# Kernel optimization log

Hardware: AMD Instinct MI355X
Metric: run time of the kernel (lower is better)

The kernel has to match this reference:

```python
import jax, jax.numpy as jnp
import numpy as np

FACTOR = 5  # init factor


def setup_inputs() -> dict:
    key = jax.random.key(0)
    k1, k2, k3, k4 = jax.random.split(key, 4)
    B, H, L, D = 4, 8, 2048, 64
    sample_k = min(FACTOR * int(np.ceil(np.log(L))), L)  # 40
    queries = jax.random.normal(k1, (B, H, L, D), dtype=jnp.float32)
    keys = jax.random.normal(k2, (B, H, L, D), dtype=jnp.float32)
    values = jax.random.normal(k3, (B, H, L, D), dtype=jnp.float32)
    index_sample = jax.random.randint(k4, (L, sample_k), 0, L)
    return {"queries": queries, "keys": keys, "values": values,
            "index_sample": index_sample}


def reference(queries, keys, values, index_sample):
    B, H, L_Q, D = queries.shape
    L_K = keys.shape[2]
    n_top = min(FACTOR * int(np.ceil(np.log(L_Q))), L_Q)

    # --- _prob_QK ---
    # Gather sampled keys per query position: [B,H,L_Q,sample_k,D]
    K_sample = keys[:, :, index_sample, :]
    # Q.unsqueeze(3) @ K_sample^T -> [B,H,L_Q,sample_k]
    Q_K_sample = jnp.einsum('bhld,bhlsd->bhls', queries, K_sample)
    # sparsity measure M = max - mean
    M = Q_K_sample.max(axis=-1) - Q_K_sample.sum(axis=-1) / L_K
    _, M_top = jax.lax.top_k(M, n_top)  # [B,H,n_top]
    # gather top queries: [B,H,n_top,D]
    Q_reduce = jnp.take_along_axis(queries, M_top[..., None], axis=2)
    # full scores for top queries: [B,H,n_top,L_K]
    scores_top = jnp.einsum('bhud,bhkd->bhuk', Q_reduce, keys)

    # --- scale ---
    scale = 1.0 / np.sqrt(D).astype(np.float32)
    scores_top = scores_top * scale

    # --- initial context (mask_flag=False): mean of V broadcast over L_Q ---
    V_mean = values.mean(axis=2)  # [B,H,D]
    context = jnp.broadcast_to(V_mean[:, :, None, :], (B, H, L_Q, D))

    # --- update context at top-query positions ---
    attn = jax.nn.softmax(scores_top, axis=-1)           # [B,H,n_top,L_K]
    ctx_update = jnp.einsum('bhuk,bhkd->bhud', attn, values)
    b_idx = jnp.arange(B)[:, None, None]
    h_idx = jnp.arange(H)[None, :, None]
    context = context.at[b_idx, h_idx, M_top].set(ctx_update)
    return context
```

## Files before the change

kernel.cpp:

```cpp
#include <hip/hip_runtime.h>
#include <math.h>

#define BH 32
#define L  2048
#define D  64
#define SK 40
#define NT 40
#define NC 16
#define CK 128
#define SCALE 0.125f

#define WS_M      0
#define WS_MTOP   262144
#define WS_VP     267264
#define WS_VM     332800
#define WS_OPART  344064
#define WS_MPART  5586944
#define WS_LPART  5668864

__global__ __launch_bounds__(256) void kM(const float* __restrict__ Q,
                                          const float* __restrict__ K,
                                          const int* __restrict__ idx,
                                          float* __restrict__ M)
{
    __shared__ int sidx[16 * SK];
    int b    = blockIdx.x;
    int xcd  = b & 7;
    int slot = b >> 3;
    int head = (slot & 3) * 8 + xcd;
    int qc   = slot >> 2;
    int wave = threadIdx.x >> 6;
    int lane = threadIdx.x & 63;
    int qq   = lane >> 4;
    int dl   = lane & 15;

    int l0 = qc * 16;
    for (int i = threadIdx.x; i < 16 * SK; i += 256)
        sidx[i] = idx[(l0 + i / SK) * SK + (i % SK)];
    __syncthreads();

    int lq  = wave * 4 + qq;
    int l   = l0 + lq;
    int qid = head * L + l;

    float4 qv = reinterpret_cast<const float4*>(Q)[(size_t)qid * 16 + dl];
    const float4* K4 = reinterpret_cast<const float4*>(K) + (size_t)head * L * 16;

    float mx = -INFINITY, sm = 0.f;
    #pragma unroll 8
    for (int s = 0; s < SK; ++s) {
        int kr = sidx[lq * SK + s];
        float4 kv = K4[(size_t)kr * 16 + dl];
        float p = qv.x * kv.x + qv.y * kv.y + qv.z * kv.z + qv.w * kv.w;
        #pragma unroll
        for (int o = 1; o < 16; o <<= 1) p += __shfl_xor(p, o, 64);
        mx = fmaxf(mx, p);
        sm += p;
    }
    if (dl == 0) M[qid] = mx - sm * (1.0f / (float)L);
}

__global__ __launch_bounds__(256) void kTop(const float* __restrict__ M, int* __restrict__ Mtop)
{
    __shared__ unsigned int keys[L];
    __shared__ int hist[256];
    __shared__ int ssum[256];
    __shared__ int bsel;
    __shared__ unsigned int pref_s;
    __shared__ int krem_s;
    __shared__ int cnt_gt, cnt_eq;
    __shared__ int eqlist[64];

    int bh = blockIdx.x;
    int t  = threadIdx.x;

    for (int i = t; i < L; i += 256) {
        unsigned int u = __float_as_uint(M[bh * L + i]);
        keys[i] = (u & 0x80000000u) ? ~u : (u | 0x80000000u);
    }
    if (t == 0) { pref_s = 0u; krem_s = NT; cnt_gt = 0; cnt_eq = 0; }
    __syncthreads();

    #pragma unroll
    for (int shift = 24; shift >= 0; shift -= 8) {
        hist[t] = 0;
        __syncthreads();
        unsigned int pref = pref_s;
        for (int i = t; i < L; i += 256) {
            unsigned int k  = keys[i];
            unsigned int hi = (shift == 24) ? 0u : (k >> (shift + 8));
            if (hi == pref) atomicAdd(&hist[(k >> shift) & 0xFF], 1);
        }
        __syncthreads();
        ssum[t] = hist[t];
        __syncthreads();
        for (int st = 1; st < 256; st <<= 1) {
            int v = (t + st < 256) ? ssum[t + st] : 0;
            __syncthreads();
            ssum[t] += v;
            __syncthreads();
        }
        int krem = krem_s;
        int excl = ssum[t] - hist[t];
        if (excl < krem && excl + hist[t] >= krem) bsel = t;
        __syncthreads();
        if (t == 0) {
            int bb = bsel;
            krem_s = krem_s - (ssum[bb] - hist[bb]);
            pref_s = (pref_s << 8) | (unsigned int)bb;
        }
        __syncthreads();
    }

    unsigned int T = pref_s;
    int krem = krem_s;
    for (int i = t; i < L; i += 256) {
        unsigned int k = keys[i];
        if (k > T) {
            int p = atomicAdd(&cnt_gt, 1);
            Mtop[bh * NT + p] = i;
        } else if (k == T) {
            int p = atomicAdd(&cnt_eq, 1);
            if (p < 64) eqlist[p] = i;
        }
    }
    __syncthreads();
    if (t == 0) {
        int base = cnt_gt;
        int m = cnt_eq < 64 ? cnt_eq : 64;
        for (int q = 0; q < krem; ++q) {
            int best = 0x7fffffff, bj = -1;
            for (int j = 0; j < m; ++j) if (eqlist[j] < best) { best = eqlist[j]; bj = j; }
            Mtop[bh * NT + base + q] = best;
            if (bj >= 0) eqlist[bj] = 0x7fffffff;
        }
    }
}

__global__ __launch_bounds__(256) void kVmean1(const float* __restrict__ V,
                                               float* __restrict__ Vp)
{
    __shared__ float red[256];
    int b  = blockIdx.x;
    int bh = b >> 3, c = b & 7;
    int dl = threadIdx.x & 63;
    int g  = threadIdx.x >> 6;
    const float* Vb = V + (size_t)bh * L * D;
    float acc = 0.f;
    int base = c * 256 + g * 64;
    for (int k = 0; k < 64; ++k) acc += Vb[(size_t)(base + k) * D + dl];
    red[threadIdx.x] = acc;
    __syncthreads();
    if (threadIdx.x < 64)
        Vp[b * 64 + dl] = red[dl] + red[64 + dl] + red[128 + dl] + red[192 + dl];
}

__global__ __launch_bounds__(64) void kVmean2(const float* __restrict__ Vp,
                                              float* __restrict__ Vm)
{
    int bh = blockIdx.x, d = threadIdx.x;
    float s = 0.f;
    #pragma unroll
    for (int c = 0; c < 8; ++c) s += Vp[(bh * 8 + c) * 64 + d];
    Vm[bh * D + d] = s * (1.0f / (float)L);
}

__global__ __launch_bounds__(256) void kFill(const float* __restrict__ Vm,
                                             float* __restrict__ out)
{
    int tid  = blockIdx.x * 256 + threadIdx.x;
    int base = tid * 4;
    int bh   = base >> 17;
    int d0   = base & (D - 1);
    float4 v = *reinterpret_cast<const float4*>(Vm + bh * D + d0);
    *reinterpret_cast<float4*>(out + base) = v;
}

__global__ __launch_bounds__(256, 2) void kAttnPart(const float* __restrict__ Q,
                                                    const float* __restrict__ K,
                                                    const float* __restrict__ V,
                                                    const int* __restrict__ Mtop,
                                                    float* __restrict__ Opart,
                                                    float* __restrict__ mpart,
                                                    float* __restrict__ lpart)
{
    __shared__ float4 KV4[CK * 16];
    __shared__ float4 Qs4[NT * 16];
    __shared__ float  S[NT * CK];
    __shared__ int    mrow[NT];
    __shared__ float  smax[NT], ssum[NT];

    int c = blockIdx.x, bh = blockIdx.y;
    int t = threadIdx.x;

    if (t < NT) mrow[t] = Mtop[bh * NT + t];
    __syncthreads();

    const float4* Qg = reinterpret_cast<const float4*>(Q) + (size_t)bh * L * 16;
    for (int i = t; i < NT * 16; i += 256) {
        int u = i >> 4, d4 = i & 15;
        Qs4[i] = Qg[(size_t)mrow[u] * 16 + d4];
    }
    const float4* Kg = reinterpret_cast<const float4*>(K) + ((size_t)bh * L + c * CK) * 16;
    for (int i = t; i < CK * 16; i += 256) {
        int j = i >> 4, d4 = i & 15;
        KV4[j * 16 + (d4 ^ (j & 15))] = Kg[i];
    }
    __syncthreads();

    {
        int wave = t >> 6, lane = t & 63;
        int jh = wave & 1, uh = wave >> 1;
        int j = jh * 64 + lane;
        float4 k4[16];
        #pragma unroll
        for (int d4 = 0; d4 < 16; ++d4) k4[d4] = KV4[j * 16 + (d4 ^ (j & 15))];
        for (int u = uh * 20; u < uh * 20 + 20; ++u) {
            float acc = 0.f;
            #pragma unroll
            for (int d4 = 0; d4 < 16; ++d4) {
                float4 q4 = Qs4[u * 16 + d4];
                acc += k4[d4].x * q4.x + k4[d4].y * q4.y
                     + k4[d4].z * q4.z + k4[d4].w * q4.w;
            }
            S[u * CK + j] = acc * SCALE;
        }
    }
    __syncthreads();

    const float4* Vg = reinterpret_cast<const float4*>(V) + ((size_t)bh * L + c * CK) * 16;
    float4 vreg[8];
    #pragma unroll
    for (int k = 0; k < 8; ++k) vreg[k] = Vg[t + k * 256];

    {
        int wave = t >> 6, lane = t & 63;
        for (int u = wave * 10; u < wave * 10 + 10; ++u) {
            float s0 = S[u * CK + lane], s1 = S[u * CK + 64 + lane];
            float m = fmaxf(s0, s1);
            #pragma unroll
            for (int o = 1; o < 64; o <<= 1) m = fmaxf(m, __shfl_xor(m, o, 64));
            float e0 = __expf(s0 - m), e1 = __expf(s1 - m);
            S[u * CK + lane] = e0; S[u * CK + 64 + lane] = e1;
            float l2 = e0 + e1;
            #pragma unroll
            for (int o = 1; o < 64; o <<= 1) l2 += __shfl_xor(l2, o, 64);
            if (lane == 0) { smax[u] = m; ssum[u] = l2; }
        }
    }
    __syncthreads();

    #pragma unroll
    for (int k = 0; k < 8; ++k) {
        int i = t + k * 256;
        int j = i >> 4, d4 = i & 15;
        KV4[j * 16 + (d4 ^ (j & 15))] = vreg[k];
    }
    __syncthreads();

    {
        int a = t >> 5, r = t & 31;
        int d4 = r >> 1, jh = r & 1;
        float4 acc[5];
        #pragma unroll
        for (int ui = 0; ui < 5; ++ui) acc[ui] = make_float4(0.f, 0.f, 0.f, 0.f);
        for (int jj = 0; jj < 64; ++jj) {
            int j = jh * 64 + jj;
            float4 v4 = KV4[j * 16 + (d4 ^ (j & 15))];
            #pragma unroll
            for (int ui = 0; ui < 5; ++ui) {
                float p = S[(a + 8 * ui) * CK + j];
                acc[ui].x += p * v4.x; acc[ui].y += p * v4.y;
                acc[ui].z += p * v4.z; acc[ui].w += p * v4.w;
            }
        }
        #pragma unroll
        for (int ui = 0; ui < 5; ++ui) {
            acc[ui].x += __shfl_xor(acc[ui].x, 1, 64);
            acc[ui].y += __shfl_xor(acc[ui].y, 1, 64);
            acc[ui].z += __shfl_xor(acc[ui].z, 1, 64);
            acc[ui].w += __shfl_xor(acc[ui].w, 1, 64);
        }
        if (jh == 0) {
            float4* Og = reinterpret_cast<float4*>(Opart) + ((size_t)(bh * NC + c) * NT) * 16;
            #pragma unroll
            for (int ui = 0; ui < 5; ++ui)
                Og[(a + 8 * ui) * 16 + d4] = acc[ui];
        }
    }
    if (t < NT) {
        mpart[(bh * NC + blockIdx.x) * NT + t] = smax[t];
        lpart[(bh * NC + blockIdx.x) * NT + t] = ssum[t];
    }
}

__global__ __launch_bounds__(64) void kCombine(const float* __restrict__ Opart,
                                               const float* __restrict__ mpart,
                                               const float* __restrict__ lpart,
                                               const int* __restrict__ Mtop,
                                               float* __restrict__ out)
{
    int u = blockIdx.x, bh = blockIdx.y, d = threadIdx.x;
    float gm = -INFINITY, den = 0.f, o = 0.f;
    for (int c = 0; c < NC; ++c) {
        int pi = (bh * NC + c) * NT + u;
        float mv = mpart[pi], lv = lpart[pi];
        float nm = fmaxf(gm, mv);
        float r1 = __expf(gm - nm), r2 = __expf(mv - nm);
        o   = o * r1 + r2 * Opart[(size_t)pi * D + d];
        den = den * r1 + r2 * lv;
        gm  = nm;
    }
    int qrow = Mtop[bh * NT + u];
    out[((size_t)bh * L + qrow) * D + d] = o / den;
}

extern "C" void kernel_launch(void* const* d_in, const int* in_sizes, int n_in,
                              void* d_out, int out_size, void* d_ws, size_t ws_size,
                              hipStream_t stream)
{
    const float* Q   = (const float*)d_in[0];
    const float* K   = (const float*)d_in[1];
    const float* V   = (const float*)d_in[2];
    const int*   idx = (const int*)d_in[3];
    float* out = (float*)d_out;

    char* ws = (char*)d_ws;
    float* M     = (float*)(ws + WS_M);
    int*   Mtop  = (int*)  (ws + WS_MTOP);
    float* Vp    = (float*)(ws + WS_VP);
    float* Vm    = (float*)(ws + WS_VM);
    float* Opart = (float*)(ws + WS_OPART);
    float* mpart = (float*)(ws + WS_MPART);
    float* lpart = (float*)(ws + WS_LPART);

    kM      <<<4096, 256, 0, stream>>>(Q, K, idx, M);
    kTop    <<<BH, 256, 0, stream>>>(M, Mtop);
    kVmean1 <<<BH * 8, 256, 0, stream>>>(V, Vp);
    kVmean2 <<<BH, 64, 0, stream>>>(Vp, Vm);
    kFill   <<<(BH * L * D) / (4 * 256), 256, 0, stream>>>(Vm, out);
    kAttnPart<<<dim3(NC, BH), 256, 0, stream>>>(Q, K, V, Mtop, Opart, mpart, lpart);
    kCombine<<<dim3(NT, BH), 64, 0, stream>>>(Opart, mpart, lpart, Mtop, out);
}
```

Before: 176.0 us.

## Fuse V-mean into scoring and top-k kernels, fold fill into attention

```diff
diff --git a/kernel.cpp b/kernel.cpp
--- a/kernel.cpp
+++ b/kernel.cpp
@@ -18,49 +18,77 @@
 #define WS_MPART  5586944
 #define WS_LPART  5668864
 
-__global__ __launch_bounds__(256) void kM(const float* __restrict__ Q,
-                                          const float* __restrict__ K,
-                                          const int* __restrict__ idx,
-                                          float* __restrict__ M)
-{
-    __shared__ int sidx[16 * SK];
-    int b    = blockIdx.x;
-    int xcd  = b & 7;
-    int slot = b >> 3;
-    int head = (slot & 3) * 8 + xcd;
-    int qc   = slot >> 2;
-    int wave = threadIdx.x >> 6;
-    int lane = threadIdx.x & 63;
-    int qq   = lane >> 4;
-    int dl   = lane & 15;
-
-    int l0 = qc * 16;
-    for (int i = threadIdx.x; i < 16 * SK; i += 256)
-        sidx[i] = idx[(l0 + i / SK) * SK + (i % SK)];
-    __syncthreads();
-
-    int lq  = wave * 4 + qq;
-    int l   = l0 + lq;
-    int qid = head * L + l;
-
-    float4 qv = reinterpret_cast<const float4*>(Q)[(size_t)qid * 16 + dl];
-    const float4* K4 = reinterpret_cast<const float4*>(K) + (size_t)head * L * 16;
-
-    float mx = -INFINITY, sm = 0.f;
-    #pragma unroll 8
-    for (int s = 0; s < SK; ++s) {
-        int kr = sidx[lq * SK + s];
-        float4 kv = K4[(size_t)kr * 16 + dl];
-        float p = qv.x * kv.x + qv.y * kv.y + qv.z * kv.z + qv.w * kv.w;
-        #pragma unroll
-        for (int o = 1; o < 16; o <<= 1) p += __shfl_xor(p, o, 64);
-        mx = fmaxf(mx, p);
-        sm += p;
-    }
-    if (dl == 0) M[qid] = mx - sm * (1.0f / (float)L);
-}
-
-__global__ __launch_bounds__(256) void kTop(const float* __restrict__ M, int* __restrict__ Mtop)
+__global__ __launch_bounds__(256) void kMV(const float* __restrict__ Q,
+                                           const float* __restrict__ K,
+                                           const float* __restrict__ V,
+                                           const int* __restrict__ idx,
+                                           float* __restrict__ M,
+                                           float* __restrict__ Vp)
+{
+    __shared__ int   sidx[64 * SK];
+    __shared__ float red[256];
+
+    int t = threadIdx.x;
+    if (blockIdx.x < 1024) {
+        int b    = blockIdx.x;
+        int xcd  = b & 7;
+        int head = ((b >> 3) & 3) * 8 + xcd;
+        int qc   = b >> 5;
+        int l0   = qc * 64;
+
+        for (int i = t; i < 64 * SK; i += 256) sidx[i] = idx[l0 * SK + i];
+        __syncthreads();
+
+        int wave = t >> 6, lane = t & 63;
+        int g  = lane >> 2;
+        int dl = lane & 3;
+        int lq = wave * 16 + g;
+        int l  = l0 + lq;
+        int qid = head * L + l;
+
+        const float4* Q4 = reinterpret_cast<const float4*>(Q);
+        float4 q0 = Q4[(size_t)qid * 16 + dl * 4 + 0];
+        float4 q1 = Q4[(size_t)qid * 16 + dl * 4 + 1];
+        float4 q2 = Q4[(size_t)qid * 16 + dl * 4 + 2];
+        float4 q3 = Q4[(size_t)qid * 16 + dl * 4 + 3];
+        const float4* Kb4 = reinterpret_cast<const float4*>(K) + (size_t)head * L * 16;
+
+        float mx = -INFINITY, sm = 0.f;
+        #pragma unroll 4
+        for (int s = 0; s < SK; ++s) {
+            int kr = sidx[lq * SK + s];
+            const float4* kp = Kb4 + (size_t)kr * 16 + dl * 4;
+            float4 k0 = kp[0], k1 = kp[1], k2 = kp[2], k3 = kp[3];
+            float p = q0.x * k0.x + q0.y * k0.y + q0.z * k0.z + q0.w * k0.w
+                    + q1.x * k1.x + q1.y * k1.y + q1.z * k1.z + q1.w * k1.w
+                    + q2.x * k2.x + q2.y * k2.y + q2.z * k2.z + q2.w * k2.w
+                    + q3.x * k3.x + q3.y * k3.y + q3.z * k3.z + q3.w * k3.w;
+            p += __shfl_xor(p, 1, 64);
+            p += __shfl_xor(p, 2, 64);
+            mx = fmaxf(mx, p);
+            sm += p;
+        }
+        if (dl == 0) M[qid] = mx - sm * (1.0f / (float)L);
+    } else {
+        int b2 = blockIdx.x - 1024;
+        int bh = b2 >> 3, c = b2 & 7;
+        int dl = t & 63;
+        int gg = t >> 6;
+        const float* Vb = V + (size_t)bh * L * D;
+        float acc = 0.f;
+        int base = c * 256 + gg * 64;
+        for (int k = 0; k < 64; ++k) acc += Vb[(size_t)(base + k) * D + dl];
+        red[t] = acc;
+        __syncthreads();
+        if (t < 64)
+            Vp[b2 * 64 + dl] = red[dl] + red[64 + dl] + red[128 + dl] + red[192 + dl];
+    }
+}
+
+__global__ __launch_bounds__(256) void kTopVm(const float* __restrict__ M,
+                                              const float* __restrict__ Vp,
+                                              int* __restrict__ Mtop,
+                                              float* __restrict__ Vm)
 {
     __shared__ unsigned int keys[L];
     __shared__ int hist[256];
@@ -73,6 +101,13 @@
 
     int bh = blockIdx.x;
     int t  = threadIdx.x;
+
+    if (t < 64) {
+        float s = 0.f;
+        #pragma unroll
+        for (int c = 0; c < 8; ++c) s += Vp[(bh * 8 + c) * 64 + t];
+        Vm[bh * D + t] = s * (1.0f / (float)L);
+    }
 
     for (int i = t; i < L; i += 256) {
         unsigned int u = __float_as_uint(M[bh * L + i]);
@@ -137,52 +172,15 @@
     }
 }
 
-__global__ __launch_bounds__(256) void kVmean1(const float* __restrict__ V,
-                                               float* __restrict__ Vp)
-{
-    __shared__ float red[256];
-    int b  = blockIdx.x;
-    int bh = b >> 3, c = b & 7;
-    int dl = threadIdx.x & 63;
-    int g  = threadIdx.x >> 6;
-    const float* Vb = V + (size_t)bh * L * D;
-    float acc = 0.f;
-    int base = c * 256 + g * 64;
-    for (int k = 0; k < 64; ++k) acc += Vb[(size_t)(base + k) * D + dl];
-    red[threadIdx.x] = acc;
-    __syncthreads();
-    if (threadIdx.x < 64)
-        Vp[b * 64 + dl] = red[dl] + red[64 + dl] + red[128 + dl] + red[192 + dl];
-}
-
-__global__ __launch_bounds__(64) void kVmean2(const float* __restrict__ Vp,
-                                              float* __restrict__ Vm)
-{
-    int bh = blockIdx.x, d = threadIdx.x;
-    float s = 0.f;
-    #pragma unroll
-    for (int c = 0; c < 8; ++c) s += Vp[(bh * 8 + c) * 64 + d];
-    Vm[bh * D + d] = s * (1.0f / (float)L);
-}
-
-__global__ __launch_bounds__(256) void kFill(const float* __restrict__ Vm,
-                                             float* __restrict__ out)
-{
-    int tid  = blockIdx.x * 256 + threadIdx.x;
-    int base = tid * 4;
-    int bh   = base >> 17;
-    int d0   = base & (D - 1);
-    float4 v = *reinterpret_cast<const float4*>(Vm + bh * D + d0);
-    *reinterpret_cast<float4*>(out + base) = v;
-}
-
 __global__ __launch_bounds__(256, 2) void kAttnPart(const float* __restrict__ Q,
                                                     const float* __restrict__ K,
                                                     const float* __restrict__ V,
                                                     const int* __restrict__ Mtop,
+                                                    const float* __restrict__ Vm,
                                                     float* __restrict__ Opart,
                                                     float* __restrict__ mpart,
-                                                    float* __restrict__ lpart)
+                                                    float* __restrict__ lpart,
+                                                    float* __restrict__ out)
 {
     __shared__ float4 KV4[CK * 16];
     __shared__ float4 Qs4[NT * 16];
@@ -192,6 +190,13 @@
 
     int c = blockIdx.x, bh = blockIdx.y;
     int t = threadIdx.x;
+
+    {
+        const float4* Vm4 = reinterpret_cast<const float4*>(Vm + bh * D);
+        float4* outB = reinterpret_cast<float4*>(out) + ((size_t)bh * L + c * CK) * 16;
+        #pragma unroll
+        for (int k = 0; k < 8; ++k) { int i = t + k * 256; outB[i] = Vm4[i & 15]; }
+    }
 
     if (t < NT) mrow[t] = Mtop[bh * NT + t];
     __syncthreads();
@@ -289,8 +294,8 @@
         }
     }
     if (t < NT) {
-        mpart[(bh * NC + blockIdx.x) * NT + t] = smax[t];
-        lpart[(bh * NC + blockIdx.x) * NT + t] = ssum[t];
+        mpart[(bh * NC + c) * NT + t] = smax[t];
+        lpart[(bh * NC + c) * NT + t] = ssum[t];
     }
 }
 
@@ -334,11 +339,8 @@
     float* mpart = (float*)(ws + WS_MPART);
     float* lpart = (float*)(ws + WS_LPART);
 
-    kM      <<<4096, 256, 0, stream>>>(Q, K, idx, M);
-    kTop    <<<BH, 256, 0, stream>>>(M, Mtop);
-    kVmean1 <<<BH * 8, 256, 0, stream>>>(V, Vp);
-    kVmean2 <<<BH, 64, 0, stream>>>(Vp, Vm);
-    kFill   <<<(BH * L * D) / (4 * 256), 256, 0, stream>>>(Vm, out);
-    kAttnPart<<<dim3(NC, BH), 256, 0, stream>>>(Q, K, V, Mtop, Opart, mpart, lpart);
-    kCombine<<<dim3(NT, BH), 64, 0, stream>>>(Opart, mpart, lpart, Mtop, out);
-}
+    kMV      <<<1280, 256, 0, stream>>>(Q, K, V, idx, M, Vp);
+    kTopVm   <<<BH, 256, 0, stream>>>(M, Vp, Mtop, Vm);
+    kAttnPart<<<dim3(NC, BH), 256, 0, stream>>>(Q, K, V, Mtop, Vm, Opart, mpart, lpart, out);
+    kCombine <<<dim3(NT, BH), 64, 0, stream>>>(Opart, mpart, lpart, Mtop, out);
+}
```

Result: slower. 179.7 us (+2.1%).
